# Kernel tuning notes

Hardware: AMD Instinct MI355X
Metric: run time of the kernel (lower is better)

Reference implementation:

```python
import jax, jax.numpy as jnp
import numpy as np
from jax import lax

NX, NY = 6, 6
NB = NX * NY            # 36 blocks
B, S = 64, 256          # batch, sample_count
EPS = 1e-6

def build_edges(nx, ny):
    edges = []
    for i in range(nx):
        for j in range(ny):
            for dx, dy in [(-1, 0), (0, -1), (0, 1), (1, 0)]:
                x, y = i + dx, j + dy
                if 0 <= x < nx and 0 <= y < ny:
                    edges.append((j * nx + i, y * nx + x))
    return np.array(edges, np.int32)   # (120, 2)

EDGES_NP = build_edges(NX, NY)
NE = len(EDGES_NP)  # 120

def setup_inputs() -> dict:
    key = jax.random.key(0)
    ks = jax.random.split(key, 24)
    f32 = jnp.float32
    d = {
        "image":      jax.random.normal(ks[0], (B, 1, 32, 32), f32),
        "edge_noise": jax.random.uniform(ks[1], (B, S, NE), f32),
        "u_s":        jax.random.uniform(ks[2], (B, S, NB), f32),
        "u_d":        jax.random.uniform(ks[3], (B, S, NB), f32),
        # CNN params (OIHW)
        "cw1": jax.random.normal(ks[4], (32, 1, 5, 5), f32) * 0.05,
        "cb1": jnp.zeros((32,), f32),
        "cw2": jax.random.normal(ks[5], (32, 32, 5, 5), f32) * 0.05,
        "cb2": jnp.zeros((32,), f32),
        "cw3": jax.random.normal(ks[6], (64, 32, 5, 5), f32) * 0.05,
        "cb3": jnp.zeros((64,), f32),
        "cw4": jax.random.normal(ks[7], (64, 64, 5, 5), f32) * 0.05,
        "cb4": jnp.zeros((64,), f32),
        # is_connected MLP
        "wc1": jax.random.normal(ks[8], (256, 256), f32) * 0.05,
        "bc1": jnp.zeros((256,), f32),
        "wc2": jax.random.normal(ks[9], (256, NE), f32) * 0.05,
        "bc2": jnp.zeros((NE,), f32),
        # is_endpoint MLP
        "we1": jax.random.normal(ks[10], (256, 256), f32) * 0.05,
        "be1": jnp.zeros((256,), f32),
        "we2": jax.random.normal(ks[11], (256, NB), f32) * 0.05,
        "be2": jnp.zeros((NB,), f32),
        "edges": jnp.asarray(EDGES_NP),  # (NE, 2) int32, constants
    }
    return d

def _conv(x, w, b):
    y = lax.conv_general_dilated(x, w, (1, 1), 'VALID',
                                 dimension_numbers=('NCHW', 'OIHW', 'NCHW'))
    return y + b[None, :, None, None]

def _pool2(x):
    return lax.reduce_window(x, -jnp.inf, lax.max, (1, 1, 2, 2), (1, 1, 2, 2), 'VALID')

def reference(image, edge_noise, u_s, u_d,
              cw1, cb1, cw2, cb2, cw3, cb3, cw4, cb4,
              wc1, bc1, wc2, bc2, we1, be1, we2, be2, edges):
    # ---- CNN feature extractor ----
    h = _conv(image, cw1, cb1)
    h = _conv(h, cw2, cb2)
    h = _pool2(h)
    h = _conv(h, cw3, cb3)
    h = _conv(h, cw4, cb4)
    h = _pool2(h)
    emb = h.reshape(h.shape[0], -1)              # (B, 256)

    # ---- heads ----
    p_conn = jax.nn.sigmoid(jax.nn.relu(emb @ wc1 + bc1) @ wc2 + bc2)   # (B, NE)
    p_ep   = jax.nn.sigmoid(jax.nn.relu(emb @ we1 + be1) @ we2 + be2)   # (B, NB)

    pc = jnp.clip(p_conn, EPS, 1.0 - EPS)
    pe = jnp.clip(p_ep, EPS, 1.0 - EPS)
    cat = pe / pe.sum(-1, keepdims=True)
    logcat = jnp.log(cat)                        # (B, NB)

    # ---- Monte-Carlo sampling (ISED blackbox) ----
    conn = (edge_noise < pc[:, None, :]).astype(pc.dtype)               # (B,S,NE) Bernoulli
    g_s = -jnp.log(-jnp.log(jnp.clip(u_s, EPS, 1.0 - EPS)))
    g_d = -jnp.log(-jnp.log(jnp.clip(u_d, EPS, 1.0 - EPS)))
    s_idx = jnp.argmax(logcat[:, None, :] + g_s, axis=-1)               # (B,S) categorical
    d_idx = jnp.argmax(logcat[:, None, :] + g_d, axis=-1)               # (B,S)

    # ---- batched BFS reachability via boolean matrix squaring ----
    oh_u = jax.nn.one_hot(edges[:, 0], NB, dtype=pc.dtype)              # (NE, NB)
    oh_v = jax.nn.one_hot(edges[:, 1], NB, dtype=pc.dtype)
    e_sym = jnp.einsum('eu,ev->euv', oh_u, oh_v) + jnp.einsum('eu,ev->evu', oh_u, oh_v)
    A = jnp.minimum(jnp.einsum('bse,euv->bsuv', conn, e_sym), 1.0)      # (B,S,36,36)

    R = jnp.minimum(A + jnp.eye(NB, dtype=A.dtype), 1.0)
    for _ in range(6):                           # (I+A)^(2^6), covers path len<=36
        R = jnp.minimum(R @ R, 1.0)
    P = jnp.minimum(A @ R, 1.0)                  # paths of length >= 1 (BFS semantics)

    Pv = jnp.take_along_axis(P, s_idx[:, :, None, None], axis=2)[:, :, 0, :]  # (B,S,36)
    exists = (jnp.take_along_axis(Pv, d_idx[:, :, None], axis=2)[:, :, 0] > 0.5).astype(pc.dtype)  # (B,S)

    # ---- sample-probability weighting (differentiable ISED estimator) ----
    logw = (conn * jnp.log(pc)[:, None, :] + (1.0 - conn) * jnp.log1p(-pc)[:, None, :]).sum(-1)
    logw = logw + jnp.take_along_axis(logcat, s_idx, axis=1) \
                + jnp.take_along_axis(logcat, d_idx, axis=1)            # (B,S)
    w = jax.nn.softmax(logw, axis=1)
    p1 = (w * exists).sum(axis=1)                # P(path exists)
    return jnp.stack([1.0 - p1, p1], axis=-1)    # (B, 2)
```

## Files before the change

### kernel.cpp

```cpp
#include <hip/hip_runtime.h>

typedef unsigned long long u64;
#define EPSF 1e-6f

__global__ __launch_bounds__(512) void k_conv1(const float* __restrict__ img,
                                               const float* __restrict__ cw1,
                                               const float* __restrict__ cb1,
                                               float* __restrict__ c1) {
  int slab = blockIdx.x, b = blockIdx.y;
  __shared__ float simg[32 * 33];
  for (int k = threadIdx.x; k < 1024; k += 512) {
    int y = k >> 5, x = k & 31;
    simg[y * 33 + x] = img[b * 1024 + k];
  }
  int half = threadIdx.x >> 8;
  int u = threadIdx.x & 255;
  int ocl = u >> 5;
  int x = u & 31;
  int oc = slab * 8 + ocl;
  int y0 = half * 14;
  float w[25];
#pragma unroll
  for (int k = 0; k < 25; ++k) w[k] = cw1[oc * 25 + k];
  float bias = cb1[oc];
  __syncthreads();
  if (x < 28) {
    float acc[5];
#pragma unroll
    for (int k = 0; k < 5; ++k) acc[k] = bias;
    float* outp = c1 + (b * 32 + oc) * 784 + x;
#pragma unroll
    for (int rr = 0; rr < 18; ++rr) {
      int r = y0 + rr;
      float in[5];
#pragma unroll
      for (int c = 0; c < 5; ++c) in[c] = simg[r * 33 + x + c];
#pragma unroll
      for (int ky = 0; ky < 5; ++ky) {
        if (rr < ky || rr - ky > 13) continue;
        int slot = (rr - ky) % 5;
#pragma unroll
        for (int kx = 0; kx < 5; ++kx)
          acc[slot] = fmaf(w[ky * 5 + kx], in[kx], acc[slot]);
      }
      if (rr >= 4) {
        int slot = (rr - 4) % 5;
        outp[(y0 + rr - 4) * 28] = acc[slot];
        acc[slot] = bias;
      }
    }
  }
}

__global__ __launch_bounds__(384) void k_conv2(const float* __restrict__ c1,
                                               const float* __restrict__ cw2,
                                               const float* __restrict__ cb2,
                                               float* __restrict__ p1w) {
  int ocq = blockIdx.x, rh = blockIdx.y, b = blockIdx.z;
  __shared__ float smem[9984];
  float* w2s = smem;
  float* sl = smem + 6400;
  int t = threadIdx.x;
  int g = t / 48, p = t % 48;
  int ocg = p / 12, row = p % 12;
  {
    const float4* src = (const float4*)(cw2 + ocq * 8 * 800);
    for (int k4 = t; k4 < 1600; k4 += 384) {
      float4 v = src[k4];
      float vv[4] = {v.x, v.y, v.z, v.w};
      int k = k4 * 4;
#pragma unroll
      for (int r = 0; r < 4; ++r) {
        int kk = k + r;
        int o = kk / 800, rest = kk % 800;
        w2s[rest * 8 + o] = vv[r];
      }
    }
  }
  float acc[2][24];
#pragma unroll
  for (int j = 0; j < 2; ++j)
#pragma unroll
    for (int c = 0; c < 24; ++c) acc[j][c] = 0.f;

  int r0 = rh * 12;
#pragma unroll
  for (int icl = 0; icl < 4; ++icl) {
    int ic = g + icl * 8;
    __syncthreads();
    {
      const float4* src = (const float4*)(c1 + (b * 32 + ic) * 784 + r0 * 28);
      float4* dst = (float4*)(sl + g * 448);
      for (int k = p; k < 112; k += 48) dst[k] = src[k];
    }
    __syncthreads();
#pragma unroll
    for (int ky = 0; ky < 5; ++ky) {
      const float4* rp = (const float4*)(sl + g * 448 + (row + ky) * 28);
      float win[28];
#pragma unroll
      for (int q = 0; q < 7; ++q) {
        float4 v = rp[q];
        win[4 * q] = v.x; win[4 * q + 1] = v.y; win[4 * q + 2] = v.z; win[4 * q + 3] = v.w;
      }
      const float* wb = w2s + (ic * 25 + ky * 5) * 8 + ocg * 2;
#pragma unroll
      for (int kx = 0; kx < 5; ++kx) {
        float2 wv = *(const float2*)(wb + kx * 8);
#pragma unroll
        for (int c = 0; c < 24; ++c) {
          acc[0][c] = fmaf(wv.x, win[c + kx], acc[0][c]);
          acc[1][c] = fmaf(wv.y, win[c + kx], acc[1][c]);
        }
      }
    }
  }
  float* buf = smem;
  __syncthreads();
  if (g >= 4) {
    float* d = buf + (g - 4) * 2304 + p * 48;
#pragma unroll
    for (int j = 0; j < 2; ++j)
#pragma unroll
      for (int c = 0; c < 24; ++c) d[j * 24 + c] = acc[j][c];
  }
  __syncthreads();
  if (g < 4) {
    const float* s = buf + g * 2304 + p * 48;
#pragma unroll
    for (int j = 0; j < 2; ++j)
#pragma unroll
      for (int c = 0; c < 24; ++c) acc[j][c] += s[j * 24 + c];
  }
  __syncthreads();
  if (g == 2 || g == 3) {
    float* d = buf + (g - 2) * 2304 + p * 48;
#pragma unroll
    for (int j = 0; j < 2; ++j)
#pragma unroll
      for (int c = 0; c < 24; ++c) d[j * 24 + c] = acc[j][c];
  }
  __syncthreads();
  if (g < 2) {
    const float* s = buf + g * 2304 + p * 48;
#pragma unroll
    for (int j = 0; j < 2; ++j)
#pragma unroll
      for (int c = 0; c < 24; ++c) acc[j][c] += s[j * 24 + c];
  }
  __syncthreads();
  if (g == 1) {
    float* d = buf + p * 48;
#pragma unroll
    for (int j = 0; j < 2; ++j)
#pragma unroll
      for (int c = 0; c < 24; ++c) d[j * 24 + c] = acc[j][c];
  }
  __syncthreads();
  float* pb = buf + 2304;
  if (g == 0) {
    const float* s = buf + p * 48;
#pragma unroll
    for (int j = 0; j < 2; ++j) {
      float bias = cb2[ocq * 8 + ocg * 2 + j];
#pragma unroll
      for (int c = 0; c < 24; ++c)
        pb[(ocg * 2 + j) * 288 + row * 24 + c] = acc[j][c] + s[j * 24 + c] + bias;
    }
  }
  __syncthreads();
  for (int k = t; k < 576; k += 384) {
    int o = k / 72, rem = k % 72;
    int py = rem / 12, px = rem % 12;
    const float* b0 = pb + o * 288 + (2 * py) * 24 + 2 * px;
    float m = fmaxf(fmaxf(b0[0], b0[1]), fmaxf(b0[24], b0[25]));
    p1w[(b * 32 + ocq * 8 + o) * 144 + (rh * 6 + py) * 12 + px] = m;
  }
}

__global__ __launch_bounds__(256) void k_conv3(const float* __restrict__ p1w,
                                               const float* __restrict__ cw3,
                                               const float* __restrict__ cb3,
                                               float* __restrict__ c3) {
  int oc8 = blockIdx.x, b = blockIdx.y;
  __shared__ float smem[11008];
  float* w3s = smem;
  float* ins = smem + 6400;
  int t = threadIdx.x;
  {
    const float4* src = (const float4*)(p1w + b * 32 * 144);
    float4* dst = (float4*)ins;
    for (int k = t; k < 1152; k += 256) dst[k] = src[k];
  }
  {
    const float4* src = (const float4*)(cw3 + oc8 * 8 * 800);
    for (int k4 = t; k4 < 1600; k4 += 256) {
      float4 v = src[k4];
      float vv[4] = {v.x, v.y, v.z, v.w};
      int k = k4 * 4;
#pragma unroll
      for (int r = 0; r < 4; ++r) {
        int kk = k + r;
        int o = kk / 800, rest = kk % 800;
        w3s[rest * 8 + o] = vv[r];
      }
    }
  }
  int g = t >> 4, p = t & 15;
  int ocg = p >> 3, row = p & 7;
  float acc[4][8];
#pragma unroll
  for (int j = 0; j < 4; ++j)
#pragma unroll
    for (int c = 0; c < 8; ++c) acc[j][c] = 0.f;
  __syncthreads();
#pragma unroll
  for (int icl = 0; icl < 2; ++icl) {
    int ic = g + icl * 16;
#pragma unroll
    for (int ky = 0; ky < 5; ++ky) {
      const float4* rp = (const float4*)(ins + ic * 144 + (row + ky) * 12);
      float win[12];
#pragma unroll
      for (int q = 0; q < 3; ++q) {
        float4 v = rp[q];
        win[4 * q] = v.x; win[4 * q + 1] = v.y; win[4 * q + 2] = v.z; win[4 * q + 3] = v.w;
      }
      const float* wb = w3s + (ic * 25 + ky * 5) * 8 + ocg * 4;
#pragma unroll
      for (int kx = 0; kx < 5; ++kx) {
        float wq[4];
        *(float4*)wq = *(const float4*)(wb + kx * 8);
#pragma unroll
        for (int c = 0; c < 8; ++c) {
#pragma unroll
          for (int j = 0; j < 4; ++j) acc[j][c] = fmaf(wq[j], win[c + kx], acc[j][c]);
        }
      }
    }
  }
  float* buf = smem;
  __syncthreads();
  if (g >= 8) {
    float* d = buf + (g - 8) * 512 + p * 32;
#pragma unroll
    for (int j = 0; j < 4; ++j)
#pragma unroll
      for (int c = 0; c < 8; ++c) d[j * 8 + c] = acc[j][c];
  }
  __syncthreads();
  if (g < 8) {
    const float* s = buf + g * 512 + p * 32;
#pragma unroll
    for (int j = 0; j < 4; ++j)
#pragma unroll
      for (int c = 0; c < 8; ++c) acc[j][c] += s[j * 8 + c];
  }
  __syncthreads();
  if (g >= 4 && g < 8) {
    float* d = buf + (g - 4) * 512 + p * 32;
#pragma unroll
    for (int j = 0; j < 4; ++j)
#pragma unroll
      for (int c = 0; c < 8; ++c) d[j * 8 + c] = acc[j][c];
  }
  __syncthreads();
  if (g < 4) {
    const float* s = buf + g * 512 + p * 32;
#pragma unroll
    for (int j = 0; j < 4; ++j)
#pragma unroll
      for (int c = 0; c < 8; ++c) acc[j][c] += s[j * 8 + c];
  }
  __syncthreads();
  if (g == 2 || g == 3) {
    float* d = buf + (g - 2) * 512 + p * 32;
#pragma unroll
    for (int j = 0; j < 4; ++j)
#pragma unroll
      for (int c = 0; c < 8; ++c) d[j * 8 + c] = acc[j][c];
  }
  __syncthreads();
  if (g < 2) {
    const float* s = buf + g * 512 + p * 32;
#pragma unroll
    for (int j = 0; j < 4; ++j)
#pragma unroll
      for (int c = 0; c < 8; ++c) acc[j][c] += s[j * 8 + c];
  }
  __syncthreads();
  if (g == 1) {
    float* d = buf + p * 32;
#pragma unroll
    for (int j = 0; j < 4; ++j)
#pragma unroll
      for (int c = 0; c < 8; ++c) d[j * 8 + c] = acc[j][c];
  }
  __syncthreads();
  if (g == 0) {
    const float* s = buf + p * 32;
#pragma unroll
    for (int j = 0; j < 4; ++j) {
      float bias = cb3[oc8 * 8 + ocg * 4 + j];
      float4 v0, v1;
      v0.x = acc[j][0] + s[j * 8 + 0] + bias; v0.y = acc[j][1] + s[j * 8 + 1] + bias;
      v0.z = acc[j][2] + s[j * 8 + 2] + bias; v0.w = acc[j][3] + s[j * 8 + 3] + bias;
      v1.x = acc[j][4] + s[j * 8 + 4] + bias; v1.y = acc[j][5] + s[j * 8 + 5] + bias;
      v1.z = acc[j][6] + s[j * 8 + 6] + bias; v1.w = acc[j][7] + s[j * 8 + 7] + bias;
      float* op = c3 + (b * 64 + oc8 * 8 + ocg * 4 + j) * 64 + row * 8;
      *(float4*)op = v0; *(float4*)(op + 4) = v1;
    }
  }
}

__global__ __launch_bounds__(256) void k_conv4(const float* __restrict__ c3,
                                               const float* __restrict__ cw4,
                                               const float* __restrict__ cb4,
                                               float* __restrict__ emb) {
  int oc8 = blockIdx.x, b = blockIdx.y;
  __shared__ float smem[17152];
  float* w4s = smem;
  float* ins = smem + 12800;
  int t = threadIdx.x;
  {
    const float4* src = (const float4*)(c3 + b * 4096);
    for (int k = t; k < 1024; k += 256) {
      int ic = k >> 4, q = k & 15;
      *(float4*)(ins + ic * 68 + q * 4) = src[k];
    }
  }
  {
    const float4* src = (const float4*)(cw4 + oc8 * 8 * 1600);
    for (int k4 = t; k4 < 3200; k4 += 256) {
      float4 v = src[k4];
      float vv[4] = {v.x, v.y, v.z, v.w};
      int k = k4 * 4;
#pragma unroll
      for (int r = 0; r < 4; ++r) {
        int kk = k + r;
        int o = kk / 1600, rest = kk % 1600;
        w4s[rest * 8 + o] = vv[r];
      }
    }
  }
  int g = t >> 3, p = t & 7;
  int ocg = p >> 2, row = p & 3;
  float acc[4][4];
#pragma unroll
  for (int j = 0; j < 4; ++j)
#pragma unroll
    for (int c = 0; c < 4; ++c) acc[j][c] = 0.f;
  __syncthreads();
#pragma unroll
  for (int icl = 0; icl < 2; ++icl) {
    int ic = g + icl * 32;
#pragma unroll
    for (int ky = 0; ky < 5; ++ky) {
      const float4* rp = (const float4*)(ins + ic * 68 + (row + ky) * 8);
      float win[8];
#pragma unroll
      for (int q = 0; q < 2; ++q) {
        float4 v = rp[q];
        win[4 * q] = v.x; win[4 * q + 1] = v.y; win[4 * q + 2] = v.z; win[4 * q + 3] = v.w;
      }
      const float* wb = w4s + (ic * 25 + ky * 5) * 8 + ocg * 4;
#pragma unroll
      for (int kx = 0; kx < 5; ++kx) {
        float wq[4];
        *(float4*)wq = *(const float4*)(wb + kx * 8);
#pragma unroll
        for (int c = 0; c < 4; ++c) {
#pragma unroll
          for (int j = 0; j < 4; ++j) acc[j][c] = fmaf(wq[j], win[c + kx], acc[j][c]);
        }
      }
    }
  }
  float* buf = smem;
#pragma unroll
  for (int half = 16; half >= 1; half >>= 1) {
    __syncthreads();
    if (g >= half && g < 2 * half) {
      float* d = buf + (g - half) * 128 + p * 16;
#pragma unroll
      for (int j = 0; j < 4; ++j)
#pragma unroll
        for (int c = 0; c < 4; ++c) d[j * 4 + c] = acc[j][c];
    }
    __syncthreads();
    if (g < half) {
      const float* s = buf + g * 128 + p * 16;
#pragma unroll
      for (int j = 0; j < 4; ++j)
#pragma unroll
        for (int c = 0; c < 4; ++c) acc[j][c] += s[j * 4 + c];
    }
  }
  float* pb = buf + 2048;
  if (g == 0) {
#pragma unroll
    for (int j = 0; j < 4; ++j) {
      float bias = cb4[oc8 * 8 + ocg * 4 + j];
#pragma unroll
      for (int c = 0; c < 4; ++c) pb[(ocg * 4 + j) * 16 + row * 4 + c] = acc[j][c] + bias;
    }
  }
  __syncthreads();
  if (t < 32) {
    int o = t >> 2, q = t & 3, py = q >> 1, px = q & 1;
    const float* b0 = pb + o * 16 + (2 * py) * 4 + 2 * px;
    float m = fmaxf(fmaxf(b0[0], b0[1]), fmaxf(b0[4], b0[5]));
    emb[b * 256 + (oc8 * 8 + o) * 4 + py * 2 + px] = m;
  }
}

__global__ __launch_bounds__(256) void k_heads(const float* __restrict__ emb,
    const float* __restrict__ wc1, const float* __restrict__ bc1,
    const float* __restrict__ wc2, const float* __restrict__ bc2,
    const float* __restrict__ we1, const float* __restrict__ be1,
    const float* __restrict__ we2, const float* __restrict__ be2,
    float* __restrict__ pcw, float* __restrict__ lpcw,
    float* __restrict__ l1mw, float* __restrict__ lcatw) {
  int head = blockIdx.x, b = blockIdx.y;
  int t = threadIdx.x;
  __shared__ float e_s[256], h_s[256];
  __shared__ float aux;
  e_s[t] = emb[b * 256 + t];
  __syncthreads();
  const float* W1 = head ? we1 : wc1;
  const float* B1 = head ? be1 : bc1;
  float s = B1[t];
  for (int i = 0; i < 256; i += 4) {
    s = fmaf(e_s[i], W1[i * 256 + t], s);
    s = fmaf(e_s[i + 1], W1[(i + 1) * 256 + t], s);
    s = fmaf(e_s[i + 2], W1[(i + 2) * 256 + t], s);
    s = fmaf(e_s[i + 3], W1[(i + 3) * 256 + t], s);
  }
  h_s[t] = fmaxf(s, 0.f);
  __syncthreads();
  int NO = head ? 36 : 120;
  const float* W2 = head ? we2 : wc2;
  const float* B2 = head ? be2 : bc2;
  if (t < NO) {
    float s2 = B2[t];
    for (int i = 0; i < 256; ++i) s2 = fmaf(h_s[i], W2[i * NO + t], s2);
    float p = 1.f / (1.f + expf(-s2));
    p = fminf(fmaxf(p, EPSF), 1.f - EPSF);
    if (head == 0) {
      pcw[b * 120 + t] = p;
      lpcw[b * 120 + t] = logf(p);
      l1mw[b * 120 + t] = log1pf(-p);
    } else {
      e_s[t] = p;
    }
  }
  if (head == 1) {
    __syncthreads();
    if (t == 0) {
      float sm = 0.f;
      for (int j2 = 0; j2 < 36; ++j2) sm += e_s[j2];
      aux = sm;
    }
    __syncthreads();
    if (t < 36) lcatw[b * 36 + t] = logf(e_s[t] / aux);
  }
}

__global__ __launch_bounds__(256) void k_mc(const float* __restrict__ enoise,
    const float* __restrict__ us, const float* __restrict__ ud,
    const int* __restrict__ edges,
    const float* __restrict__ pcw, const float* __restrict__ lpcw,
    const float* __restrict__ l1mw, const float* __restrict__ lcatw,
    float* __restrict__ out) {
  int b = blockIdx.x, t = threadIdx.x;
  __shared__ __align__(16) float pc_s[120];
  __shared__ __align__(16) float lpc_s[120];
  __shared__ __align__(16) float l1m_s[120];
  __shared__ __align__(16) float lcat_s[36];
  __shared__ __align__(16) int einfo[120];
  __shared__ float red_s[256];
  if (t < 120) {
    pc_s[t] = pcw[b * 120 + t];
    lpc_s[t] = lpcw[b * 120 + t];
    l1m_s[t] = l1mw[b * 120 + t];
    int u = edges[2 * t], v = edges[2 * t + 1];
    int d = v - u;
    int isV = (d == 6 || d == -6) ? 1 : 0;
    int pos = d > 0 ? u : v;
    einfo[t] = pos | (isV << 6);
  }
  if (t < 36) lcat_s[t] = lcatw[b * 36 + t];
  __syncthreads();

  float logw = 0.f;
  u64 H = 0, V = 0;
  {
    const float4* np = (const float4*)(enoise + ((size_t)(b * 256 + t)) * 120);
#pragma unroll
    for (int q = 0; q < 30; ++q) {
      float4 nz = np[q];
      float4 p4 = ((const float4*)pc_s)[q];
      float4 lp4 = ((const float4*)lpc_s)[q];
      float4 lm4 = ((const float4*)l1m_s)[q];
      int4 e4 = ((const int4*)einfo)[q];
      float nv[4] = {nz.x, nz.y, nz.z, nz.w};
      float pv[4] = {p4.x, p4.y, p4.z, p4.w};
      float lv[4] = {lp4.x, lp4.y, lp4.z, lp4.w};
      float mv[4] = {lm4.x, lm4.y, lm4.z, lm4.w};
      int ev[4] = {e4.x, e4.y, e4.z, e4.w};
#pragma unroll
      for (int r = 0; r < 4; ++r) {
        bool conn = nv[r] < pv[r];
        logw += conn ? lv[r] : mv[r];
        if (conn) {
          u64 bit = 1ull << (ev[r] & 63);
          if (ev[r] & 64) V |= bit; else H |= bit;
        }
      }
    }
  }
  int si = 0, di = 0;
  {
    const float4* up = (const float4*)(us + ((size_t)(b * 256 + t)) * 36);
    float best = -1e30f;
#pragma unroll
    for (int q = 0; q < 9; ++q) {
      float4 uv = up[q];
      float4 lc4 = ((const float4*)lcat_s)[q];
      float vv[4] = {uv.x, uv.y, uv.z, uv.w};
      float lc[4] = {lc4.x, lc4.y, lc4.z, lc4.w};
#pragma unroll
      for (int r = 0; r < 4; ++r) {
        float u = fminf(fmaxf(vv[r], EPSF), 1.f - EPSF);
        float gq = -logf(-logf(u));
        float val = lc[r] + gq;
        if (val > best) { best = val; si = q * 4 + r; }
      }
    }
  }
  {
    const float4* up = (const float4*)(ud + ((size_t)(b * 256 + t)) * 36);
    float best = -1e30f;
#pragma unroll
    for (int q = 0; q < 9; ++q) {
      float4 uv = up[q];
      float4 lc4 = ((const float4*)lcat_s)[q];
      float vv[4] = {uv.x, uv.y, uv.z, uv.w};
      float lc[4] = {lc4.x, lc4.y, lc4.z, lc4.w};
#pragma unroll
      for (int r = 0; r < 4; ++r) {
        float u = fminf(fmaxf(vv[r], EPSF), 1.f - EPSF);
        float gq = -logf(-logf(u));
        float val = lc[r] + gq;
        if (val > best) { best = val; di = q * 4 + r; }
      }
    }
  }
  logw += lcat_s[si] + lcat_s[di];

  u64 comp = 1ull << si;
  while (true) {
    u64 prev = comp;
    comp |= ((comp & H) << 1) | ((comp >> 1) & H);
    comp |= ((comp & V) << 6) | ((comp >> 6) & V);
    if (comp == prev) break;
  }
  float ex;
  if (si == di) ex = (comp != (1ull << si)) ? 1.f : 0.f;
  else ex = ((comp >> di) & 1ull) ? 1.f : 0.f;

  red_s[t] = logw; __syncthreads();
  for (int off = 128; off > 0; off >>= 1) {
    if (t < off) red_s[t] = fmaxf(red_s[t], red_s[t + off]);
    __syncthreads();
  }
  float m = red_s[0]; __syncthreads();
  float evx = expf(logw - m);
  red_s[t] = evx; __syncthreads();
  for (int off = 128; off > 0; off >>= 1) {
    if (t < off) red_s[t] += red_s[t + off];
    __syncthreads();
  }
  float den = red_s[0]; __syncthreads();
  red_s[t] = evx * ex; __syncthreads();
  for (int off = 128; off > 0; off >>= 1) {
    if (t < off) red_s[t] += red_s[t + off];
    __syncthreads();
  }
  if (t == 0) {
    float p1v = red_s[0] / den;
    out[b * 2] = 1.f - p1v;
    out[b * 2 + 1] = p1v;
  }
}

extern "C" void kernel_launch(void* const* d_in, const int* in_sizes, int n_in,
                              void* d_out, int out_size, void* d_ws, size_t ws_size,
                              hipStream_t stream) {
  const float* image = (const float*)d_in[0];
  const float* enoise = (const float*)d_in[1];
  const float* us = (const float*)d_in[2];
  const float* udn = (const float*)d_in[3];
  const float* cw1 = (const float*)d_in[4];
  const float* cb1 = (const float*)d_in[5];
  const float* cw2 = (const float*)d_in[6];
  const float* cb2 = (const float*)d_in[7];
  const float* cw3 = (const float*)d_in[8];
  const float* cb3 = (const float*)d_in[9];
  const float* cw4 = (const float*)d_in[10];
  const float* cb4 = (const float*)d_in[11];
  const float* wc1 = (const float*)d_in[12];
  const float* bc1 = (const float*)d_in[13];
  const float* wc2 = (const float*)d_in[14];
  const float* bc2 = (const float*)d_in[15];
  const float* we1 = (const float*)d_in[16];
  const float* be1 = (const float*)d_in[17];
  const float* we2 = (const float*)d_in[18];
  const float* be2 = (const float*)d_in[19];
  const int* edges = (const int*)d_in[20];

  float* ws = (float*)d_ws;
  float* c1 = ws;
  float* p1w = ws + 1605632;
  float* c3 = ws + 1900544;
  float* emb = ws + 2162688;
  float* pcw = ws + 2179072;
  float* lpcw = ws + 2186752;
  float* l1mw = ws + 2194432;
  float* lcatw = ws + 2202112;
  float* outp = (float*)d_out;

  k_conv1<<<dim3(4, 64), dim3(512), 0, stream>>>(image, cw1, cb1, c1);
  k_conv2<<<dim3(4, 2, 64), dim3(384), 0, stream>>>(c1, cw2, cb2, p1w);
  k_conv3<<<dim3(8, 64), dim3(256), 0, stream>>>(p1w, cw3, cb3, c3);
  k_conv4<<<dim3(8, 64), dim3(256), 0, stream>>>(c3, cw4, cb4, emb);
  k_heads<<<dim3(2, 64), dim3(256), 0, stream>>>(emb, wc1, bc1, wc2, bc2,
                                                 we1, be1, we2, be2,
                                                 pcw, lpcw, l1mw, lcatw);
  k_mc<<<dim3(64), dim3(256), 0, stream>>>(enoise, us, udn, edges,
                                           pcw, lpcw, l1mw, lcatw, outp);
}
```

Before: 134.5 us.

## Restructure conv2 to one wave per output channel with 3x3 register tiles

Conv2 is rewritten so each block stages all 32 input channels of one image in shared memory, and each wave computes one output channel. Each lane produces a 3x3 output tile, and the weights are read as wave-uniform values from global memory. This removes the split across input channels and its multi-step shared-memory reduction with many barriers, as well as the two row-halves grid dimension. The trade-offs are about 116KB of shared memory per block, which limits occupancy to one block per CU, and half as many blocks, so there is less parallelism.

```diff
diff --git a/kernel.cpp b/kernel.cpp
--- a/kernel.cpp
+++ b/kernel.cpp
@@ -52,129 +52,70 @@
   }
 }
 
-__global__ __launch_bounds__(384) void k_conv2(const float* __restrict__ c1,
+__global__ __launch_bounds__(512) void k_conv2(const float* __restrict__ c1,
                                                const float* __restrict__ cw2,
                                                const float* __restrict__ cb2,
                                                float* __restrict__ p1w) {
-  int ocq = blockIdx.x, rh = blockIdx.y, b = blockIdx.z;
-  __shared__ float smem[9984];
-  float* w2s = smem;
-  float* sl = smem + 6400;
+  int ocq = blockIdx.x, b = blockIdx.y;
+  __shared__ float smem[29696];
+  float* sInp = smem;
+  float* pb = smem + 25088;
   int t = threadIdx.x;
-  int g = t / 48, p = t % 48;
-  int ocg = p / 12, row = p % 12;
-  {
-    const float4* src = (const float4*)(cw2 + ocq * 8 * 800);
-    for (int k4 = t; k4 < 1600; k4 += 384) {
-      float4 v = src[k4];
-      float vv[4] = {v.x, v.y, v.z, v.w};
-      int k = k4 * 4;
-#pragma unroll
-      for (int r = 0; r < 4; ++r) {
-        int kk = k + r;
-        int o = kk / 800, rest = kk % 800;
-        w2s[rest * 8 + o] = vv[r];
-      }
-    }
-  }
-  float acc[2][24];
-#pragma unroll
-  for (int j = 0; j < 2; ++j)
-#pragma unroll
-    for (int c = 0; c < 24; ++c) acc[j][c] = 0.f;
-
-  int r0 = rh * 12;
-#pragma unroll
-  for (int icl = 0; icl < 4; ++icl) {
-    int ic = g + icl * 8;
-    __syncthreads();
-    {
-      const float4* src = (const float4*)(c1 + (b * 32 + ic) * 784 + r0 * 28);
-      float4* dst = (float4*)(sl + g * 448);
-      for (int k = p; k < 112; k += 48) dst[k] = src[k];
-    }
-    __syncthreads();
-#pragma unroll
-    for (int ky = 0; ky < 5; ++ky) {
-      const float4* rp = (const float4*)(sl + g * 448 + (row + ky) * 28);
-      float win[28];
-#pragma unroll
-      for (int q = 0; q < 7; ++q) {
-        float4 v = rp[q];
-        win[4 * q] = v.x; win[4 * q + 1] = v.y; win[4 * q + 2] = v.z; win[4 * q + 3] = v.w;
-      }
-      const float* wb = w2s + (ic * 25 + ky * 5) * 8 + ocg * 2;
-#pragma unroll
-      for (int kx = 0; kx < 5; ++kx) {
-        float2 wv = *(const float2*)(wb + kx * 8);
-#pragma unroll
-        for (int c = 0; c < 24; ++c) {
-          acc[0][c] = fmaf(wv.x, win[c + kx], acc[0][c]);
-          acc[1][c] = fmaf(wv.y, win[c + kx], acc[1][c]);
+  {
+    const float4* src = (const float4*)(c1 + (size_t)b * 32 * 784);
+    float4* dst = (float4*)sInp;
+    for (int k = t; k < 6272; k += 512) dst[k] = src[k];
+  }
+  int w = __builtin_amdgcn_readfirstlane(t >> 6);
+  int l = t & 63;
+  int py = l >> 3, px = l & 7;
+  int oc = ocq * 8 + w;
+  const float* wrow = cw2 + (size_t)oc * 800;
+  float acc[3][3];
+#pragma unroll
+  for (int i = 0; i < 3; ++i)
+#pragma unroll
+    for (int j = 0; j < 3; ++j) acc[i][j] = 0.f;
+  __syncthreads();
+
+  const float* base0 = sInp + 3 * py * 28 + 3 * px;
+  for (int ic = 0; ic < 32; ++ic) {
+    float w25[25];
+    const float* wr = wrow + ic * 25;
+#pragma unroll
+    for (int k = 0; k < 25; ++k) w25[k] = wr[k];
+    const float* base = base0 + ic * 784;
+#pragma unroll
+    for (int rr = 0; rr < 7; ++rr) {
+      float win[7];
+#pragma unroll
+      for (int m = 0; m < 7; ++m) win[m] = base[rr * 28 + m];
+#pragma unroll
+      for (int i = 0; i < 3; ++i) {
+        if (i > rr || rr - i > 4) continue;
+        int ky = rr - i;
+#pragma unroll
+        for (int kx = 0; kx < 5; ++kx) {
+#pragma unroll
+          for (int j = 0; j < 3; ++j)
+            acc[i][j] = fmaf(w25[ky * 5 + kx], win[j + kx], acc[i][j]);
         }
       }
     }
   }
-  float* buf = smem;
-  __syncthreads();
-  if (g >= 4) {
-    float* d = buf + (g - 4) * 2304 + p * 48;
-#pragma unroll
-    for (int j = 0; j < 2; ++j)
-#pragma unroll
-      for (int c = 0; c < 24; ++c) d[j * 24 + c] = acc[j][c];
-  }
-  __syncthreads();
-  if (g < 4) {
-    const float* s = buf + g * 2304 + p * 48;
-#pragma unroll
-    for (int j = 0; j < 2; ++j)
-#pragma unroll
-      for (int c = 0; c < 24; ++c) acc[j][c] += s[j * 24 + c];
-  }
-  __syncthreads();
-  if (g == 2 || g == 3) {
-    float* d = buf + (g - 2) * 2304 + p * 48;
-#pragma unroll
-    for (int j = 0; j < 2; ++j)
-#pragma unroll
-      for (int c = 0; c < 24; ++c) d[j * 24 + c] = acc[j][c];
-  }
-  __syncthreads();
-  if (g < 2) {
-    const float* s = buf + g * 2304 + p * 48;
-#pragma unroll
-    for (int j = 0; j < 2; ++j)
-#pragma unroll
-      for (int c = 0; c < 24; ++c) acc[j][c] += s[j * 24 + c];
-  }
-  __syncthreads();
-  if (g == 1) {
-    float* d = buf + p * 48;
-#pragma unroll
-    for (int j = 0; j < 2; ++j)
-#pragma unroll
-      for (int c = 0; c < 24; ++c) d[j * 24 + c] = acc[j][c];
-  }
-  __syncthreads();
-  float* pb = buf + 2304;
-  if (g == 0) {
-    const float* s = buf + p * 48;
-#pragma unroll
-    for (int j = 0; j < 2; ++j) {
-      float bias = cb2[ocq * 8 + ocg * 2 + j];
-#pragma unroll
-      for (int c = 0; c < 24; ++c)
-        pb[(ocg * 2 + j) * 288 + row * 24 + c] = acc[j][c] + s[j * 24 + c] + bias;
-    }
-  }
-  __syncthreads();
-  for (int k = t; k < 576; k += 384) {
-    int o = k / 72, rem = k % 72;
-    int py = rem / 12, px = rem % 12;
-    const float* b0 = pb + o * 288 + (2 * py) * 24 + 2 * px;
+  float bias = cb2[oc];
+  float* pbw = pb + w * 576 + 3 * py * 24 + 3 * px;
+#pragma unroll
+  for (int i = 0; i < 3; ++i)
+#pragma unroll
+    for (int j = 0; j < 3; ++j) pbw[i * 24 + j] = acc[i][j] + bias;
+  __syncthreads();
+  for (int k = t; k < 1152; k += 512) {
+    int o = k / 144, rem = k % 144;
+    int PY = rem / 12, PX = rem % 12;
+    const float* b0 = pb + o * 576 + (2 * PY) * 24 + 2 * PX;
     float m = fmaxf(fmaxf(b0[0], b0[1]), fmaxf(b0[24], b0[25]));
-    p1w[(b * 32 + ocq * 8 + o) * 144 + (rh * 6 + py) * 12 + px] = m;
+    p1w[((size_t)b * 32 + ocq * 8 + o) * 144 + PY * 12 + PX] = m;
   }
 }
 
@@ -631,7 +572,7 @@
   float* outp = (float*)d_out;
 
   k_conv1<<<dim3(4, 64), dim3(512), 0, stream>>>(image, cw1, cb1, c1);
-  k_conv2<<<dim3(4, 2, 64), dim3(384), 0, stream>>>(c1, cw2, cb2, p1w);
+  k_conv2<<<dim3(4, 64), dim3(512), 0, stream>>>(c1, cw2, cb2, p1w);
   k_conv3<<<dim3(8, 64), dim3(256), 0, stream>>>(p1w, cw3, cb3, c3);
   k_conv4<<<dim3(8, 64), dim3(256), 0, stream>>>(c3, cw4, cb4, emb);
   k_heads<<<dim3(2, 64), dim3(256), 0, stream>>>(emb, wc1, bc1, wc2, bc2,
```

New measurement: 127.0 us. 1.06x faster.
